# Kernel optimization log

Measured on AMD Instinct MI355X. Metric: run time of the kernel, lower is better.

The kernel has to match this reference:

```python
import jax, jax.numpy as jnp
import numpy as np

B, T, E, D, G = 64, 64, 2048, 4096, 8
H3 = 3 * D  # gru projects deter -> 3*deter (reset, cand, update)
EPS = 1e-4  # Norm default eps


def _rms(x, scale):
    # Norm impl='rms': x * rsqrt(mean(x^2, -1) + eps) * scale
    return x * (jax.lax.rsqrt((x * x).mean(-1, keepdims=True) + EPS) * scale)


def setup_inputs() -> dict:
    key = jax.random.key(0)
    ks = jax.random.split(key, 4)
    x = jax.random.normal(ks[0], (B, T, E), jnp.float32)
    deter0 = jax.random.normal(ks[1], (B, D), jnp.float32)
    # dense in-projection: concat(deter, x) -> D, rms norm + silu
    W_in = jax.random.normal(ks[2], (D + E, D), jnp.float32) * (1.0 / np.sqrt(D + E))
    b_in = jnp.zeros((D,), jnp.float32)
    scale_in = jnp.ones((D,), jnp.float32)
    # BlockLinear D -> 3D with G groups; weight (G, D/G, 3D/G), per-block rms scales
    W_blk = jax.random.normal(ks[3], (G, D // G, H3 // G), jnp.float32) * (1.0 / np.sqrt(D // G))
    b_blk = jnp.zeros((H3,), jnp.float32)
    scale_blk = jnp.ones((G, H3 // G), jnp.float32)
    return dict(x=x, deter0=deter0, W_in=W_in, b_in=b_in, scale_in=scale_in,
                W_blk=W_blk, b_blk=b_blk, scale_blk=scale_blk)


def reference(x, deter0, W_in, b_in, scale_in, W_blk, b_blk, scale_blk):
    def step(deter, x_t):
        h = jnp.concatenate([deter, x_t], -1)                # [B, D+E]
        y = jax.nn.silu(_rms(h @ W_in + b_in, scale_in))     # [B, D]
        # block-diagonal GEMM: '...ki,kio->...ko' as in BlockLinear._layer
        z = jnp.einsum('bgi,gio->bgo', y.reshape(B, G, D // G), W_blk)
        z = z.reshape(B, H3) + b_blk
        # block_norm=True: per-block rms over each of the G contiguous chunks
        z = _rms(z.reshape(B, G, H3 // G), scale_blk).reshape(B, H3)
        reset, cand, update = jnp.split(z, 3, -1)
        reset = jax.nn.sigmoid(reset)
        cand = jnp.tanh(reset * cand)
        update = jax.nn.sigmoid(update - 1.0)
        deter = update * cand + (1.0 - update) * deter
        return deter, deter

    _, deters = jax.lax.scan(step, deter0, jnp.swapaxes(x, 0, 1))  # scan over T
    return jnp.swapaxes(deters, 0, 1)  # [B, T, D]
```

## Files before the change

kernel.cpp:

```cpp
#include <hip/hip_runtime.h>

typedef unsigned short u16;
typedef unsigned int u32;
typedef __bf16 bfx8 __attribute__((ext_vector_type(8)));
typedef float f32x4 __attribute__((ext_vector_type(4)));

constexpr int BB = 64;
constexpr int TT = 64;
constexpr int EE = 2048;
constexpr int DD = 4096;
constexpr int GG = 8;
constexpr int H3 = 3 * DD;
constexpr int CH = H3 / GG;
constexpr float EPSf = 1e-4f;

static __device__ __forceinline__ u16 f2bf(float f) {
  u32 u = __builtin_bit_cast(u32, f);
  u32 r = (u + 0x7fffu + ((u >> 16) & 1u)) >> 16;
  return (u16)r;
}


__global__ void __launch_bounds__(256) k_f2b(const float* __restrict__ in,
                                             u16* __restrict__ out, int n4) {
  int i = blockIdx.x * 256 + threadIdx.x;
  int stride = gridDim.x * 256;
  for (; i < n4; i += stride) {
    float4 v = ((const float4*)in)[i];
    uint2 o;
    o.x = (u32)f2bf(v.x) | ((u32)f2bf(v.y) << 16);
    o.y = (u32)f2bf(v.z) | ((u32)f2bf(v.w) << 16);
    ((uint2*)out)[i] = o;
  }
}

__global__ void __launch_bounds__(256) k_initdet(const float* __restrict__ d0,
                                                 float* __restrict__ dF,
                                                 u16* __restrict__ dB, int n4) {
  int i = blockIdx.x * 256 + threadIdx.x;
  if (i < n4) {
    float4 v = ((const float4*)d0)[i];
    ((float4*)dF)[i] = v;
    uint2 o;
    o.x = (u32)f2bf(v.x) | ((u32)f2bf(v.y) << 16);
    o.y = (u32)f2bf(v.z) | ((u32)f2bf(v.w) << 16);
    ((uint2*)dB)[i] = o;
  }
}

__global__ void __launch_bounds__(256) k_transpose_f2b(const float* __restrict__ in,
                                                       u16* __restrict__ out,
                                                       int R, int C) {
  __shared__ float tile[32][33];
  size_t base = (size_t)blockIdx.z * R * C;
  in += base; out += base;
  int tx = threadIdx.x & 31, ty = threadIdx.x >> 5;
  int r0 = blockIdx.y * 32, c0 = blockIdx.x * 32;
#pragma unroll
  for (int i = 0; i < 4; i++) {
    int rr = ty * 4 + i;
    tile[rr][tx] = in[(size_t)(r0 + rr) * C + (c0 + tx)];
  }
  __syncthreads();
#pragma unroll
  for (int i = 0; i < 4; i++) {
    int cc = ty * 4 + i;
    out[(size_t)(c0 + cc) * R + (r0 + tx)] = f2bf(tile[tx][cc]);
  }
}


template<int BM, int BN, int WR, int WC>
__global__ void __launch_bounds__(256) k_gemm(
    const u16* __restrict__ A, int lda,
    const u16* __restrict__ B, int ldb,
    float* __restrict__ C, int ldc,
    const float* __restrict__ bias,
    int K) {
  constexpr int BK = 64, LS = BK + 8;
  constexpr int WTM = BM / WR, WTN = BN / WC, MF = WTM / 16, NF = WTN / 16;
  __shared__ u16 As[BM * LS];
  __shared__ u16 Bs[BN * LS];
  const int tid = threadIdx.x;
  const int m0 = blockIdx.y * BM, n0 = blockIdx.x * BN;
  const int w = tid >> 6, lane = tid & 63;
  const int wr = w / WC, wc = w % WC;
  const int lr = lane & 15, lk = (lane >> 4) * 8;

  f32x4 acc[MF][NF] = {};

  for (int kt = 0; kt < K; kt += BK) {
#pragma unroll
    for (int c = tid; c < BM * 8; c += 256) {
      int row = c >> 3, cc = c & 7;
      *(uint4*)&As[row * LS + cc * 8] =
          *(const uint4*)(A + (size_t)(m0 + row) * lda + kt + cc * 8);
    }
#pragma unroll
    for (int c = tid; c < BN * 8; c += 256) {
      int row = c >> 3, cc = c & 7;
      *(uint4*)&Bs[row * LS + cc * 8] =
          *(const uint4*)(B + (size_t)(n0 + row) * ldb + kt + cc * 8);
    }
    __syncthreads();
#pragma unroll
    for (int kk = 0; kk < BK; kk += 32) {
      bfx8 av[MF], bv[NF];
#pragma unroll
      for (int mi = 0; mi < MF; mi++)
        av[mi] = *(const bfx8*)&As[(wr * WTM + mi * 16 + lr) * LS + kk + lk];
#pragma unroll
      for (int ni = 0; ni < NF; ni++)
        bv[ni] = *(const bfx8*)&Bs[(wc * WTN + ni * 16 + lr) * LS + kk + lk];
#pragma unroll
      for (int mi = 0; mi < MF; mi++)
#pragma unroll
        for (int ni = 0; ni < NF; ni++)
          acc[mi][ni] = __builtin_amdgcn_mfma_f32_16x16x32_bf16(av[mi], bv[ni], acc[mi][ni], 0, 0, 0);
    }
    __syncthreads();
  }

  const int rq = (lane >> 4) * 4;
#pragma unroll
  for (int mi = 0; mi < MF; mi++) {
#pragma unroll
    for (int ni = 0; ni < NF; ni++) {
      int n = n0 + wc * WTN + ni * 16 + lr;
      float bias_v = bias ? bias[n] : 0.f;
#pragma unroll
      for (int r = 0; r < 4; r++) {
        int m = m0 + wr * WTM + mi * 16 + rq + r;
        C[(size_t)m * ldc + n] = acc[mi][ni][r] + bias_v;
      }
    }
  }
}

__global__ void __launch_bounds__(256) kA(const u16* __restrict__ dB,
                                          const u16* __restrict__ WT,
                                          float* __restrict__ part) {
  constexpr int LS = 72;
  __shared__ u16 As[64 * LS];
  __shared__ u16 Bs[64 * LS];
  const int tid = threadIdx.x;
  const int n0 = blockIdx.x * 64;
  const int k0 = blockIdx.y * 512;
  const int w = tid >> 6, lane = tid & 63;
  const int lr = lane & 15, lk = (lane >> 4) * 8, rq = (lane >> 4) * 4;
  const int srow = tid >> 2, sc = (tid & 3) * 8;
  const u16* Arow = dB + (size_t)srow * DD + k0 + sc;
  const u16* Brow = WT + (size_t)(n0 + srow) * (DD + EE) + k0 + sc;

  f32x4 acc[4] = {};
  for (int kt = 0; kt < 512; kt += 64) {
    *(uint4*)&As[srow * LS + sc]      = *(const uint4*)(Arow + kt);
    *(uint4*)&As[srow * LS + sc + 32] = *(const uint4*)(Arow + kt + 32);
    *(uint4*)&Bs[srow * LS + sc]      = *(const uint4*)(Brow + kt);
    *(uint4*)&Bs[srow * LS + sc + 32] = *(const uint4*)(Brow + kt + 32);
    __syncthreads();
#pragma unroll
    for (int kk = 0; kk < 64; kk += 32) {
      bfx8 av = *(const bfx8*)&As[(w * 16 + lr) * LS + kk + lk];
#pragma unroll
      for (int ni = 0; ni < 4; ni++) {
        bfx8 bv = *(const bfx8*)&Bs[(ni * 16 + lr) * LS + kk + lk];
        acc[ni] = __builtin_amdgcn_mfma_f32_16x16x32_bf16(av, bv, acc[ni], 0, 0, 0);
      }
    }
    __syncthreads();
  }
  float* P = part + (size_t)blockIdx.y * BB * DD;
#pragma unroll
  for (int ni = 0; ni < 4; ni++)
#pragma unroll
    for (int r = 0; r < 4; r++)
      P[(size_t)(w * 16 + rq + r) * DD + n0 + ni * 16 + lr] = acc[ni][r];
}

__global__ void __launch_bounds__(256) kB(const float* __restrict__ part,
                                          const float* __restrict__ Xproj,
                                          const float* __restrict__ scale_in,
                                          u16* __restrict__ ybf, int t) {
  const int b = blockIdx.x, tid = threadIdx.x;
  const int w = tid >> 6, lane = tid & 63;
  __shared__ float sred[4];
  const float* xp = Xproj + ((size_t)b * TT + t) * DD;
  const float* pb = part + (size_t)b * DD;
  float4 v[4];
  float ss = 0.f;
#pragma unroll
  for (int j = 0; j < 4; j++) {
    const int col = j * 1024 + tid * 4;
    float4 a = *(const float4*)(xp + col);
#pragma unroll
    for (int kc = 0; kc < 8; kc++) {
      float4 p = *(const float4*)(pb + (size_t)kc * BB * DD + col);
      a.x += p.x; a.y += p.y; a.z += p.z; a.w += p.w;
    }
    v[j] = a;
    ss += a.x * a.x + a.y * a.y + a.z * a.z + a.w * a.w;
  }
#pragma unroll
  for (int o = 32; o > 0; o >>= 1) ss += __shfl_down(ss, o);
  if (lane == 0) sred[w] = ss;
  __syncthreads();
  const float r = rsqrtf((sred[0] + sred[1] + sred[2] + sred[3]) / (float)DD + EPSf);
#pragma unroll
  for (int j = 0; j < 4; j++) {
    const int col = j * 1024 + tid * 4;
    float4 sc4 = *(const float4*)(scale_in + col);
    float y0 = v[j].x * r * sc4.x, y1 = v[j].y * r * sc4.y;
    float y2 = v[j].z * r * sc4.z, y3 = v[j].w * r * sc4.w;
    y0 = y0 / (1.f + __expf(-y0)); y1 = y1 / (1.f + __expf(-y1));
    y2 = y2 / (1.f + __expf(-y2)); y3 = y3 / (1.f + __expf(-y3));
    uint2 o;
    o.x = (u32)f2bf(y0) | ((u32)f2bf(y1) << 16);
    o.y = (u32)f2bf(y2) | ((u32)f2bf(y3) << 16);
    *(uint2*)(ybf + (size_t)b * DD + col) = o;
  }
}

__global__ void __launch_bounds__(256) kC(const u16* __restrict__ ybf,
                                          const u16* __restrict__ WbT,
                                          const float* __restrict__ b_blk,
                                          float* __restrict__ zbuf,
                                          float* __restrict__ zsq) {
  constexpr int LS = 72;
  __shared__ u16 As[64 * LS];
  __shared__ u16 Bs[64 * LS];
  const int tid = threadIdx.x;
  const int wg = blockIdx.x;
  const int n0g = wg * 64;
  const int g = n0g / CH, nl = n0g % CH;
  const int w = tid >> 6, lane = tid & 63;
  const int lr = lane & 15, lk = (lane >> 4) * 8, rq = (lane >> 4) * 4;
  const int srow = tid >> 2, sc = (tid & 3) * 8;
  const u16* Arow = ybf + (size_t)srow * DD + g * (DD / GG) + sc;
  const u16* Brow = WbT + ((size_t)g * CH + nl + srow) * (DD / GG) + sc;

  f32x4 acc[4] = {};
  for (int kt = 0; kt < DD / GG; kt += 64) {
    *(uint4*)&As[srow * LS + sc]      = *(const uint4*)(Arow + kt);
    *(uint4*)&As[srow * LS + sc + 32] = *(const uint4*)(Arow + kt + 32);
    *(uint4*)&Bs[srow * LS + sc]      = *(const uint4*)(Brow + kt);
    *(uint4*)&Bs[srow * LS + sc + 32] = *(const uint4*)(Brow + kt + 32);
    __syncthreads();
#pragma unroll
    for (int kk = 0; kk < 64; kk += 32) {
      bfx8 av = *(const bfx8*)&As[(w * 16 + lr) * LS + kk + lk];
#pragma unroll
      for (int ni = 0; ni < 4; ni++) {
        bfx8 bv = *(const bfx8*)&Bs[(ni * 16 + lr) * LS + kk + lk];
        acc[ni] = __builtin_amdgcn_mfma_f32_16x16x32_bf16(av, bv, acc[ni], 0, 0, 0);
      }
    }
    __syncthreads();
  }
  float sq[4] = {0.f, 0.f, 0.f, 0.f};
#pragma unroll
  for (int ni = 0; ni < 4; ni++) {
    const int n = n0g + ni * 16 + lr;
    const float bias_v = b_blk[n];
#pragma unroll
    for (int r = 0; r < 4; r++) {
      const float zv = acc[ni][r] + bias_v;
      zbuf[(size_t)(w * 16 + rq + r) * H3 + n] = zv;
      sq[r] += zv * zv;
    }
  }
#pragma unroll
  for (int o = 1; o < 16; o <<= 1) {
#pragma unroll
    for (int r = 0; r < 4; r++) sq[r] += __shfl_xor(sq[r], o);
  }
  if (lr == 0) {
#pragma unroll
    for (int r = 0; r < 4; r++) zsq[(size_t)wg * 64 + w * 16 + rq + r] = sq[r];
  }
}

__global__ void __launch_bounds__(256) kD(const float* __restrict__ zbuf,
                                          const float* __restrict__ zsq,
                                          const float* __restrict__ sblk,
                                          float* __restrict__ dF,
                                          u16* __restrict__ dB,
                                          float* __restrict__ out, int t) {
  const int wg = blockIdx.x, tid = threadIdx.x;
  const int b = wg >> 2, s = wg & 3;
  __shared__ float sred[8];
  if (tid < 8) {
    float ssq = 0.f;
    const int j0 = tid * 24;
#pragma unroll
    for (int j = 0; j < 24; j++) ssq += zsq[(size_t)(j0 + j) * 64 + b];
    sred[tid] = rsqrtf(ssq / (float)CH + EPSf);
  }
  __syncthreads();
  const int d0 = s * 1024 + tid * 4;
  const float* zr = zbuf + (size_t)b * H3;
  float4 z0 = *(const float4*)(zr + d0);
  float4 z1 = *(const float4*)(zr + DD + d0);
  float4 z2 = *(const float4*)(zr + 2 * DD + d0);
  float4 dold = *(const float4*)(dF + (size_t)b * DD + d0);
  const float rsA = sred[d0 / CH];
  const float rsB = sred[(DD + d0) / CH];
  const float rsC = sred[(2 * DD + d0) / CH];
  float dn[4];
  const float* z0p = (const float*)&z0;
  const float* z1p = (const float*)&z1;
  const float* z2p = (const float*)&z2;
  const float* dop = (const float*)&dold;
#pragma unroll
  for (int e = 0; e < 4; e++) {
    const int dd = d0 + e;
    const float a0 = z0p[e] * rsA * sblk[dd];
    const float a1 = z1p[e] * rsB * sblk[DD + dd];
    const float a2 = z2p[e] * rsC * sblk[2 * DD + dd];
    const float reset = 1.f / (1.f + __expf(-a0));
    const float cand = tanhf(reset * a1);
    const float upd = 1.f / (1.f + __expf(-(a2 - 1.f)));
    dn[e] = upd * cand + (1.f - upd) * dop[e];
  }
  *(float4*)(dF + (size_t)b * DD + d0) = make_float4(dn[0], dn[1], dn[2], dn[3]);
  uint2 o;
  o.x = (u32)f2bf(dn[0]) | ((u32)f2bf(dn[1]) << 16);
  o.y = (u32)f2bf(dn[2]) | ((u32)f2bf(dn[3]) << 16);
  *(uint2*)(dB + (size_t)b * DD + d0) = o;
  *(float4*)(out + ((size_t)b * TT + t) * DD + d0) = make_float4(dn[0], dn[1], dn[2], dn[3]);
}


extern "C" void kernel_launch(void* const* d_in, const int* in_sizes, int n_in,
                              void* d_out, int out_size, void* d_ws, size_t ws_size,
                              hipStream_t stream) {
  (void)in_sizes; (void)n_in; (void)out_size; (void)ws_size;
  const float* x         = (const float*)d_in[0];
  const float* deter0    = (const float*)d_in[1];
  const float* W_in      = (const float*)d_in[2];
  const float* b_in      = (const float*)d_in[3];
  const float* scale_in  = (const float*)d_in[4];
  const float* W_blk     = (const float*)d_in[5];
  const float* b_blk     = (const float*)d_in[6];
  const float* scale_blk = (const float*)d_in[7];
  float* out = (float*)d_out;

  char* ws = (char*)d_ws;
  size_t off = 0;
  auto alloc = [&](size_t bytes) -> void* {
    void* p = ws + off;
    off += (bytes + 255) & ~(size_t)255;
    return p;
  };
  u16*   WT    = (u16*)alloc((size_t)DD * (DD + EE) * 2);
  u16*   WbT   = (u16*)alloc((size_t)GG * CH * (DD / GG) * 2);
  float* Xproj = (float*)alloc((size_t)BB * TT * DD * 4);
  float* dF    = (float*)alloc((size_t)BB * DD * 4);
  u16*   dB    = (u16*)alloc((size_t)BB * DD * 2);
  char* scratch = (char*)alloc((size_t)BB * TT * EE * 2);
  u16*   xbf  = (u16*)scratch;
  float* part = (float*)scratch;
  size_t o2 = (size_t)8 * BB * DD * 4;
  u16*   ybf  = (u16*)(scratch + o2);
  o2 += (size_t)BB * DD * 2;
  float* zbuf = (float*)(scratch + o2);
  o2 += (size_t)BB * H3 * 4;
  float* zsq  = (float*)(scratch + o2);

  k_f2b<<<dim3(2048), dim3(256), 0, stream>>>(x, xbf, BB * TT * EE / 4);
  k_transpose_f2b<<<dim3(DD / 32, (DD + EE) / 32, 1), dim3(256), 0, stream>>>(W_in, WT, DD + EE, DD);
  k_transpose_f2b<<<dim3(CH / 32, (DD / GG) / 32, GG), dim3(256), 0, stream>>>(W_blk, WbT, DD / GG, CH);
  k_initdet<<<dim3(BB * DD / 4 / 256), dim3(256), 0, stream>>>(deter0, dF, dB, BB * DD / 4);

  k_gemm<128, 128, 2, 2><<<dim3(DD / 128, BB * TT / 128, 1), dim3(256), 0, stream>>>(
      xbf, EE,
      WT + DD, DD + EE,
      Xproj, DD,
      b_in,
      EE);

  for (int t = 0; t < TT; t++) {
    kA<<<dim3(64, 8), dim3(256), 0, stream>>>(dB, WT, part);
    kB<<<dim3(BB), dim3(256), 0, stream>>>(part, Xproj, scale_in, ybf, t);
    kC<<<dim3(192), dim3(256), 0, stream>>>(ybf, WbT, b_blk, zbuf, zsq);
    kD<<<dim3(256), dim3(256), 0, stream>>>(zbuf, zsq, scale_blk, dF, dB, out, t);
  }
}
```

Baseline: 1.965 ms.

## Double-buffer GEMM tiles, store Xproj as bf16, and retile the recurrent K-split

```diff
diff --git a/kernel.cpp b/kernel.cpp
--- a/kernel.cpp
+++ b/kernel.cpp
@@ -18,6 +18,9 @@
   u32 u = __builtin_bit_cast(u32, f);
   u32 r = (u + 0x7fffu + ((u >> 16) & 1u)) >> 16;
   return (u16)r;
+}
+static __device__ __forceinline__ float bf2f(u16 h) {
+  return __builtin_bit_cast(float, (u32)h << 16);
 }
 
 
@@ -69,166 +72,215 @@
   }
 }
 
-
-template<int BM, int BN, int WR, int WC>
-__global__ void __launch_bounds__(256) k_gemm(
-    const u16* __restrict__ A, int lda,
-    const u16* __restrict__ B, int ldb,
-    float* __restrict__ C, int ldc,
-    const float* __restrict__ bias,
-    int K) {
-  constexpr int BK = 64, LS = BK + 8;
-  constexpr int WTM = BM / WR, WTN = BN / WC, MF = WTM / 16, NF = WTN / 16;
-  __shared__ u16 As[BM * LS];
-  __shared__ u16 Bs[BN * LS];
+constexpr int P1_LS = 72;
+constexpr int P1_BUF = 128 * P1_LS;
+
+__global__ void __launch_bounds__(256) k_p1(const u16* __restrict__ A,
+                                            const u16* __restrict__ B,
+                                            const float* __restrict__ bias,
+                                            u16* __restrict__ C) {
+  __shared__ u16 As[2 * P1_BUF];
+  __shared__ u16 Bs[2 * P1_BUF];
   const int tid = threadIdx.x;
-  const int m0 = blockIdx.y * BM, n0 = blockIdx.x * BN;
+  const int m0 = blockIdx.y * 128, n0 = blockIdx.x * 128;
   const int w = tid >> 6, lane = tid & 63;
-  const int wr = w / WC, wc = w % WC;
-  const int lr = lane & 15, lk = (lane >> 4) * 8;
-
-  f32x4 acc[MF][NF] = {};
-
-  for (int kt = 0; kt < K; kt += BK) {
-#pragma unroll
-    for (int c = tid; c < BM * 8; c += 256) {
-      int row = c >> 3, cc = c & 7;
-      *(uint4*)&As[row * LS + cc * 8] =
-          *(const uint4*)(A + (size_t)(m0 + row) * lda + kt + cc * 8);
-    }
-#pragma unroll
-    for (int c = tid; c < BN * 8; c += 256) {
-      int row = c >> 3, cc = c & 7;
-      *(uint4*)&Bs[row * LS + cc * 8] =
-          *(const uint4*)(B + (size_t)(n0 + row) * ldb + kt + cc * 8);
+  const int wr = w >> 1, wc = w & 1;
+  const int lr = lane & 15, lk = (lane >> 4) * 8, rq = (lane >> 4) * 4;
+  const int srow = tid >> 3, scol = (tid & 7) * 8;
+  const u16* Ag = A + (size_t)(m0 + srow) * EE + scol;
+  const u16* Bg = B + (size_t)(n0 + srow) * (DD + EE) + scol;
+
+  f32x4 acc[4][4] = {};
+  uint4 ra[4], rb[4];
+#pragma unroll
+  for (int i = 0; i < 4; i++) {
+    ra[i] = *(const uint4*)(Ag + (size_t)32 * i * EE);
+    rb[i] = *(const uint4*)(Bg + (size_t)32 * i * (DD + EE));
+  }
+
+  for (int kt = 0; kt < 32; ++kt) {
+    const int p = kt & 1;
+    u16* ab = As + p * P1_BUF;
+    u16* bb = Bs + p * P1_BUF;
+#pragma unroll
+    for (int i = 0; i < 4; i++) {
+      *(uint4*)&ab[(srow + 32 * i) * P1_LS + scol] = ra[i];
+      *(uint4*)&bb[(srow + 32 * i) * P1_LS + scol] = rb[i];
     }
     __syncthreads();
-#pragma unroll
-    for (int kk = 0; kk < BK; kk += 32) {
-      bfx8 av[MF], bv[NF];
-#pragma unroll
-      for (int mi = 0; mi < MF; mi++)
-        av[mi] = *(const bfx8*)&As[(wr * WTM + mi * 16 + lr) * LS + kk + lk];
-#pragma unroll
-      for (int ni = 0; ni < NF; ni++)
-        bv[ni] = *(const bfx8*)&Bs[(wc * WTN + ni * 16 + lr) * LS + kk + lk];
-#pragma unroll
-      for (int mi = 0; mi < MF; mi++)
-#pragma unroll
-        for (int ni = 0; ni < NF; ni++)
+    if (kt < 31) {
+      const int ko = (kt + 1) * 64;
+#pragma unroll
+      for (int i = 0; i < 4; i++) {
+        ra[i] = *(const uint4*)(Ag + (size_t)32 * i * EE + ko);
+        rb[i] = *(const uint4*)(Bg + (size_t)32 * i * (DD + EE) + ko);
+      }
+    }
+#pragma unroll
+    for (int kk = 0; kk < 64; kk += 32) {
+      bfx8 av[4], bv[4];
+#pragma unroll
+      for (int mi = 0; mi < 4; mi++)
+        av[mi] = *(const bfx8*)&ab[(wr * 64 + mi * 16 + lr) * P1_LS + kk + lk];
+#pragma unroll
+      for (int ni = 0; ni < 4; ni++)
+        bv[ni] = *(const bfx8*)&bb[(wc * 64 + ni * 16 + lr) * P1_LS + kk + lk];
+#pragma unroll
+      for (int mi = 0; mi < 4; mi++)
+#pragma unroll
+        for (int ni = 0; ni < 4; ni++)
           acc[mi][ni] = __builtin_amdgcn_mfma_f32_16x16x32_bf16(av[mi], bv[ni], acc[mi][ni], 0, 0, 0);
     }
-    __syncthreads();
-  }
-
-  const int rq = (lane >> 4) * 4;
-#pragma unroll
-  for (int mi = 0; mi < MF; mi++) {
-#pragma unroll
-    for (int ni = 0; ni < NF; ni++) {
-      int n = n0 + wc * WTN + ni * 16 + lr;
-      float bias_v = bias ? bias[n] : 0.f;
+  }
+
+#pragma unroll
+  for (int mi = 0; mi < 4; mi++) {
+#pragma unroll
+    for (int ni = 0; ni < 4; ni++) {
+      const int n = n0 + wc * 64 + ni * 16 + lr;
+      const float bias_v = bias[n];
 #pragma unroll
       for (int r = 0; r < 4; r++) {
-        int m = m0 + wr * WTM + mi * 16 + rq + r;
-        C[(size_t)m * ldc + n] = acc[mi][ni][r] + bias_v;
+        const int m = m0 + wr * 64 + mi * 16 + rq + r;
+        C[(size_t)m * DD + n] = f2bf(acc[mi][ni][r] + bias_v);
       }
     }
   }
 }
 
-__global__ void __launch_bounds__(256) kA(const u16* __restrict__ dB,
+constexpr int LSA = 136;
+constexpr int ABUF = 64 * LSA;
+
+__global__ void __launch_bounds__(512) kA(const u16* __restrict__ dB,
                                           const u16* __restrict__ WT,
                                           float* __restrict__ part) {
-  constexpr int LS = 72;
-  __shared__ u16 As[64 * LS];
-  __shared__ u16 Bs[64 * LS];
+  __shared__ u16 As[2 * ABUF];
+  __shared__ u16 Bs[2 * ABUF];
   const int tid = threadIdx.x;
   const int n0 = blockIdx.x * 64;
-  const int k0 = blockIdx.y * 512;
+  const int k0 = blockIdx.y * 1024;
   const int w = tid >> 6, lane = tid & 63;
+  const int wr = w >> 1, wc = w & 1;
   const int lr = lane & 15, lk = (lane >> 4) * 8, rq = (lane >> 4) * 4;
-  const int srow = tid >> 2, sc = (tid & 3) * 8;
-  const u16* Arow = dB + (size_t)srow * DD + k0 + sc;
-  const u16* Brow = WT + (size_t)(n0 + srow) * (DD + EE) + k0 + sc;
-
-  f32x4 acc[4] = {};
-  for (int kt = 0; kt < 512; kt += 64) {
-    *(uint4*)&As[srow * LS + sc]      = *(const uint4*)(Arow + kt);
-    *(uint4*)&As[srow * LS + sc + 32] = *(const uint4*)(Arow + kt + 32);
-    *(uint4*)&Bs[srow * LS + sc]      = *(const uint4*)(Brow + kt);
-    *(uint4*)&Bs[srow * LS + sc + 32] = *(const uint4*)(Brow + kt + 32);
+  const int r0s = tid >> 4, s0 = (tid & 15) * 8;
+  const int r1s = r0s + 32;
+  const u16* Ag0 = dB + (size_t)r0s * DD + k0 + s0;
+  const u16* Ag1 = dB + (size_t)r1s * DD + k0 + s0;
+  const u16* Bg0 = WT + (size_t)(n0 + r0s) * (DD + EE) + k0 + s0;
+  const u16* Bg1 = WT + (size_t)(n0 + r1s) * (DD + EE) + k0 + s0;
+  const int d0 = r0s * LSA + s0, d1 = r1s * LSA + s0;
+
+  f32x4 acc[2] = {};
+  uint4 ra0 = *(const uint4*)(Ag0);
+  uint4 ra1 = *(const uint4*)(Ag1);
+  uint4 rb0 = *(const uint4*)(Bg0);
+  uint4 rb1 = *(const uint4*)(Bg1);
+
+  for (int kt = 0; kt < 8; ++kt) {
+    const int p = kt & 1;
+    u16* ab = As + p * ABUF;
+    u16* bb = Bs + p * ABUF;
+    *(uint4*)&ab[d0] = ra0;
+    *(uint4*)&ab[d1] = ra1;
+    *(uint4*)&bb[d0] = rb0;
+    *(uint4*)&bb[d1] = rb1;
     __syncthreads();
-#pragma unroll
-    for (int kk = 0; kk < 64; kk += 32) {
-      bfx8 av = *(const bfx8*)&As[(w * 16 + lr) * LS + kk + lk];
-#pragma unroll
-      for (int ni = 0; ni < 4; ni++) {
-        bfx8 bv = *(const bfx8*)&Bs[(ni * 16 + lr) * LS + kk + lk];
+    if (kt < 7) {
+      const int ko = (kt + 1) * 128;
+      ra0 = *(const uint4*)(Ag0 + ko);
+      ra1 = *(const uint4*)(Ag1 + ko);
+      rb0 = *(const uint4*)(Bg0 + ko);
+      rb1 = *(const uint4*)(Bg1 + ko);
+    }
+#pragma unroll
+    for (int kk = 0; kk < 128; kk += 32) {
+      bfx8 av = *(const bfx8*)&ab[(wr * 16 + lr) * LSA + kk + lk];
+#pragma unroll
+      for (int ni = 0; ni < 2; ni++) {
+        bfx8 bv = *(const bfx8*)&bb[(wc * 32 + ni * 16 + lr) * LSA + kk + lk];
         acc[ni] = __builtin_amdgcn_mfma_f32_16x16x32_bf16(av, bv, acc[ni], 0, 0, 0);
       }
     }
-    __syncthreads();
-  }
-  float* P = part + (size_t)blockIdx.y * BB * DD;
-#pragma unroll
-  for (int ni = 0; ni < 4; ni++)
+  }
+
+  float* Pp = part + (size_t)blockIdx.y * BB * DD;
+#pragma unroll
+  for (int ni = 0; ni < 2; ni++)
 #pragma unroll
     for (int r = 0; r < 4; r++)
-      P[(size_t)(w * 16 + rq + r) * DD + n0 + ni * 16 + lr] = acc[ni][r];
+      Pp[(size_t)(wr * 16 + rq + r) * DD + n0 + wc * 32 + ni * 16 + lr] = acc[ni][r];
 }
 
 __global__ void __launch_bounds__(256) kB(const float* __restrict__ part,
-                                          const float* __restrict__ Xproj,
+                                          const u16* __restrict__ Xproj,
                                           const float* __restrict__ scale_in,
                                           u16* __restrict__ ybf, int t) {
   const int b = blockIdx.x, tid = threadIdx.x;
   const int w = tid >> 6, lane = tid & 63;
   __shared__ float sred[4];
-  const float* xp = Xproj + ((size_t)b * TT + t) * DD;
-  const float* pb = part + (size_t)b * DD;
-  float4 v[4];
+  const u16* xp = Xproj + ((size_t)b * TT + t) * DD + tid * 16;
+  const float* pb = part + (size_t)b * DD + tid * 16;
+  float v[16];
+  uint4 x0 = *(const uint4*)(xp);
+  uint4 x1 = *(const uint4*)(xp + 8);
+#pragma unroll
+  for (int j = 0; j < 8; j++) v[j] = bf2f(((const u16*)&x0)[j]);
+#pragma unroll
+  for (int j = 0; j < 8; j++) v[8 + j] = bf2f(((const u16*)&x1)[j]);
+#pragma unroll
+  for (int kc = 0; kc < 4; kc++) {
+    const float* p = pb + (size_t)kc * BB * DD;
+#pragma unroll
+    for (int j4 = 0; j4 < 4; j4++) {
+      float4 q = *(const float4*)(p + j4 * 4);
+      v[j4 * 4 + 0] += q.x; v[j4 * 4 + 1] += q.y;
+      v[j4 * 4 + 2] += q.z; v[j4 * 4 + 3] += q.w;
+    }
+  }
   float ss = 0.f;
 #pragma unroll
-  for (int j = 0; j < 4; j++) {
-    const int col = j * 1024 + tid * 4;
-    float4 a = *(const float4*)(xp + col);
-#pragma unroll
-    for (int kc = 0; kc < 8; kc++) {
-      float4 p = *(const float4*)(pb + (size_t)kc * BB * DD + col);
-      a.x += p.x; a.y += p.y; a.z += p.z; a.w += p.w;
-    }
-    v[j] = a;
-    ss += a.x * a.x + a.y * a.y + a.z * a.z + a.w * a.w;
-  }
+  for (int j = 0; j < 16; j++) ss += v[j] * v[j];
 #pragma unroll
   for (int o = 32; o > 0; o >>= 1) ss += __shfl_down(ss, o);
   if (lane == 0) sred[w] = ss;
   __syncthreads();
   const float r = rsqrtf((sred[0] + sred[1] + sred[2] + sred[3]) / (float)DD + EPSf);
+  const float* sc = scale_in + tid * 16;
+  uint2 o0, o1;
+  u32* po = (u32*)&o0;
 #pragma unroll
   for (int j = 0; j < 4; j++) {
-    const int col = j * 1024 + tid * 4;
-    float4 sc4 = *(const float4*)(scale_in + col);
-    float y0 = v[j].x * r * sc4.x, y1 = v[j].y * r * sc4.y;
-    float y2 = v[j].z * r * sc4.z, y3 = v[j].w * r * sc4.w;
-    y0 = y0 / (1.f + __expf(-y0)); y1 = y1 / (1.f + __expf(-y1));
-    y2 = y2 / (1.f + __expf(-y2)); y3 = y3 / (1.f + __expf(-y3));
-    uint2 o;
-    o.x = (u32)f2bf(y0) | ((u32)f2bf(y1) << 16);
-    o.y = (u32)f2bf(y2) | ((u32)f2bf(y3) << 16);
-    *(uint2*)(ybf + (size_t)b * DD + col) = o;
-  }
-}
+    float a = v[2 * j] * r * sc[2 * j];
+    float bq = v[2 * j + 1] * r * sc[2 * j + 1];
+    a = a / (1.f + __expf(-a)); bq = bq / (1.f + __expf(-bq));
+    po[j & 1] = (u32)f2bf(a) | ((u32)f2bf(bq) << 16);
+    if (j == 1) *(uint2*)(ybf + (size_t)b * DD + tid * 16) = o0;
+  }
+  *(uint2*)(ybf + (size_t)b * DD + tid * 16 + 4) = o0;
+  u32 pk[8];
+#pragma unroll
+  for (int j = 0; j < 8; j++) {
+    float a = v[2 * j] * r * sc[2 * j];
+    float bq = v[2 * j + 1] * r * sc[2 * j + 1];
+    a = a / (1.f + __expf(-a)); bq = bq / (1.f + __expf(-bq));
+    pk[j] = (u32)f2bf(a) | ((u32)f2bf(bq) << 16);
+  }
+  uint4 w0 = make_uint4(pk[0], pk[1], pk[2], pk[3]);
+  uint4 w1 = make_uint4(pk[4], pk[5], pk[6], pk[7]);
+  *(uint4*)(ybf + (size_t)b * DD + tid * 16) = w0;
+  *(uint4*)(ybf + (size_t)b * DD + tid * 16 + 8) = w1;
+}
+
+constexpr int LSC2 = 72;
+constexpr int CBUF = 64 * LSC2;
 
 __global__ void __launch_bounds__(256) kC(const u16* __restrict__ ybf,
                                           const u16* __restrict__ WbT,
                                           const float* __restrict__ b_blk,
                                           float* __restrict__ zbuf,
                                           float* __restrict__ zsq) {
-  constexpr int LS = 72;
-  __shared__ u16 As[64 * LS];
-  __shared__ u16 Bs[64 * LS];
+  __shared__ u16 As[2 * CBUF];
+  __shared__ u16 Bs[2 * CBUF];
   const int tid = threadIdx.x;
   const int wg = blockIdx.x;
   const int n0g = wg * 64;
@@ -238,25 +290,41 @@
   const int srow = tid >> 2, sc = (tid & 3) * 8;
   const u16* Arow = ybf + (size_t)srow * DD + g * (DD / GG) + sc;
   const u16* Brow = WbT + ((size_t)g * CH + nl + srow) * (DD / GG) + sc;
+  const int dA = srow * LSC2 + sc;
 
   f32x4 acc[4] = {};
-  for (int kt = 0; kt < DD / GG; kt += 64) {
-    *(uint4*)&As[srow * LS + sc]      = *(const uint4*)(Arow + kt);
-    *(uint4*)&As[srow * LS + sc + 32] = *(const uint4*)(Arow + kt + 32);
-    *(uint4*)&Bs[srow * LS + sc]      = *(const uint4*)(Brow + kt);
-    *(uint4*)&Bs[srow * LS + sc + 32] = *(const uint4*)(Brow + kt + 32);
+  uint4 ra0 = *(const uint4*)(Arow);
+  uint4 ra1 = *(const uint4*)(Arow + 32);
+  uint4 rb0 = *(const uint4*)(Brow);
+  uint4 rb1 = *(const uint4*)(Brow + 32);
+
+  for (int kt = 0; kt < 8; ++kt) {
+    const int p = kt & 1;
+    u16* ab = As + p * CBUF;
+    u16* bb = Bs + p * CBUF;
+    *(uint4*)&ab[dA] = ra0;
+    *(uint4*)&ab[dA + 32] = ra1;
+    *(uint4*)&bb[dA] = rb0;
+    *(uint4*)&bb[dA + 32] = rb1;
     __syncthreads();
+    if (kt < 7) {
+      const int ko = (kt + 1) * 64;
+      ra0 = *(const uint4*)(Arow + ko);
+      ra1 = *(const uint4*)(Arow + ko + 32);
+      rb0 = *(const uint4*)(Brow + ko);
+      rb1 = *(const uint4*)(Brow + ko + 32);
+    }
 #pragma unroll
     for (int kk = 0; kk < 64; kk += 32) {
-      bfx8 av = *(const bfx8*)&As[(w * 16 + lr) * LS + kk + lk];
+      bfx8 av = *(const bfx8*)&ab[(w * 16 + lr) * LSC2 + kk + lk];
 #pragma unroll
       for (int ni = 0; ni < 4; ni++) {
-        bfx8 bv = *(const bfx8*)&Bs[(ni * 16 + lr) * LS + kk + lk];
+        bfx8 bv = *(const bfx8*)&bb[(ni * 16 + lr) * LSC2 + kk + lk];
         acc[ni] = __builtin_amdgcn_mfma_f32_16x16x32_bf16(av, bv, acc[ni], 0, 0, 0);
       }
     }
-    __syncthreads();
-  }
+  }
+
   float sq[4] = {0.f, 0.f, 0.f, 0.f};
 #pragma unroll
   for (int ni = 0; ni < 4; ni++) {
@@ -354,13 +422,13 @@
   };
   u16*   WT    = (u16*)alloc((size_t)DD * (DD + EE) * 2);
   u16*   WbT   = (u16*)alloc((size_t)GG * CH * (DD / GG) * 2);
-  float* Xproj = (float*)alloc((size_t)BB * TT * DD * 4);
+  u16*   Xproj = (u16*)alloc((size_t)BB * TT * DD * 2);
   float* dF    = (float*)alloc((size_t)BB * DD * 4);
   u16*   dB    = (u16*)alloc((size_t)BB * DD * 2);
   char* scratch = (char*)alloc((size_t)BB * TT * EE * 2);
   u16*   xbf  = (u16*)scratch;
   float* part = (float*)scratch;
-  size_t o2 = (size_t)8 * BB * DD * 4;
+  size_t o2 = (size_t)4 * BB * DD * 4;
   u16*   ybf  = (u16*)(scratch + o2);
   o2 += (size_t)BB * DD * 2;
   float* zbuf = (float*)(scratch + o2);
@@ -372,15 +440,11 @@
   k_transpose_f2b<<<dim3(CH / 32, (DD / GG) / 32, GG), dim3(256), 0, stream>>>(W_blk, WbT, DD / GG, CH);
   k_initdet<<<dim3(BB * DD / 4 / 256), dim3(256), 0, stream>>>(deter0, dF, dB, BB * DD / 4);
 
-  k_gemm<128, 128, 2, 2><<<dim3(DD / 128, BB * TT / 128, 1), dim3(256), 0, stream>>>(
-      xbf, EE,
-      WT + DD, DD + EE,
-      Xproj, DD,
-      b_in,
-      EE);
+  k_p1<<<dim3(DD / 128, BB * TT / 128), dim3(256), 0, stream>>>(
+      xbf, WT + DD, b_in, Xproj);
 
   for (int t = 0; t < TT; t++) {
-    kA<<<dim3(64, 8), dim3(256), 0, stream>>>(dB, WT, part);
+    kA<<<dim3(64, 4), dim3(512), 0, stream>>>(dB, WT, part);
     kB<<<dim3(BB), dim3(256), 0, stream>>>(part, Xproj, scale_in, ybf, t);
     kC<<<dim3(192), dim3(256), 0, stream>>>(ybf, WbT, b_blk, zbuf, zsq);
     kD<<<dim3(256), dim3(256), 0, stream>>>(zbuf, zsq, scale_blk, dF, dB, out, t);
```

Result: no change. 1.999 ms (+1.8%).
